# Optimization experiments

Measured on AMD Instinct MI355X. Metric: run time of the kernel, lower is better.

Reference implementation:

```python
import jax, jax.numpy as jnp
import numpy as np

NQ, NT, NA = 10000, 50000, 50000
E_GR, E_LT, E_SIM, E_COMP, E_GEN = 50000, 50000, 80000, 100000, 50000
HID, NH, HC, DOT, NL = 512, 4, 128, 256, 2
NEG_SLOPE = 0.2  # PyG GATv2Conv default negative_slope


def _gatv2(x_src, x_dst, src, dst, Wl, bl, Wr, br, att, bias, n_dst):
    # GATv2: x_j = lin_l(x_src), x_i = lin_r(x_dst); e = att . leaky_relu(x_i + x_j)
    xl = (x_src @ Wl + bl).reshape(-1, NH, HC)   # [Ns,H,C]
    xr = (x_dst @ Wr + br).reshape(-1, NH, HC)   # [Nd,H,C]
    m = jax.nn.leaky_relu(xl[src] + xr[dst], NEG_SLOPE)      # [E,H,C]
    logits = jnp.einsum('ehc,hc->eh', m, att)                # [E,H]
    lmax = jax.lax.stop_gradient(jax.ops.segment_max(logits, dst, num_segments=n_dst))
    lmax = jnp.where(jnp.isfinite(lmax), lmax, 0.0)
    ex = jnp.exp(logits - lmax[dst])
    denom = jax.ops.segment_sum(ex, dst, num_segments=n_dst)
    alpha = ex / (denom[dst] + 1e-16)                        # softmax over incoming edges
    out = jax.ops.segment_sum(xl[src] * alpha[:, :, None], dst, num_segments=n_dst)
    return out.reshape(n_dst, NH * HC) + bias


def _layernorm(x, g, b):
    mu = x.mean(-1, keepdims=True)
    var = ((x - mu) ** 2).mean(-1, keepdims=True)
    return (x - mu) / jnp.sqrt(var + 1e-5) * g + b


def _forward(xq, xt, xa, answer_features,
             qp_W, qp_b, tp_W, tp_b, ap_W, ap_b,
             afp_W1, afp_b1, afp_W2, afp_b2,
             conv_Wl, conv_bl, conv_Wr, conv_br, conv_att, conv_bias,
             qh_W, qh_b, qh_g, qh_beta, rh_W, rh_b, rh_g, rh_beta, score_bias,
             ei_gr, ei_lt, ei_sim, ei_comp, ei_gen):
    hq = xq @ qp_W + qp_b
    ht = xt @ tp_W + tp_b
    ha = xa @ ap_W + ap_b
    # add_self_loops=True only for ('query','similar_to','query')
    loops = jnp.arange(NQ, dtype=ei_sim.dtype)
    sim_src = jnp.concatenate([ei_sim[0], loops])
    sim_dst = jnp.concatenate([ei_sim[1], loops])
    for l in range(NL):
        P = lambda r: (conv_Wl[l, r], conv_bl[l, r], conv_Wr[l, r], conv_br[l, r], conv_att[l, r], conv_bias[l, r])
        o_gr = _gatv2(hq, ht, ei_gr[0], ei_gr[1], *P(0), NT)          # query -> think
        o_rgr = _gatv2(ht, hq, ei_gr[1], ei_gr[0], *P(1), NQ)         # think -> query (rev)
        o_lt = _gatv2(ht, ha, ei_lt[0], ei_lt[1], *P(2), NA)          # think -> answer
        o_rlt = _gatv2(ha, ht, ei_lt[1], ei_lt[0], *P(3), NT)         # answer -> think (rev)
        o_sim = _gatv2(hq, hq, sim_src, sim_dst, *P(4), NQ)           # query -> query
        o_cmp = _gatv2(ht, ht, ei_comp[0], ei_comp[1], *P(5), NT)     # think -> think
        # HeteroConv aggr='mean' across relations per destination type, then relu
        hq = jax.nn.relu((o_rgr + o_sim) / 2.0)
        ht = jax.nn.relu((o_gr + o_rlt + o_cmp) / 3.0)
        ha = jax.nn.relu(o_lt)
    q_emb = hq[ei_gen[0]]
    a_emb = ha[ei_gen[1]]
    t_emb = ht[ei_gen[1]]  # faithful to source: think indexed with answer-side index
    af_emb = jax.nn.relu(answer_features @ afp_W1 + afp_b1) @ afp_W2 + afp_b2
    q = _layernorm(q_emb @ qh_W + qh_b, qh_g, qh_beta)
    r = _layernorm(jnp.concatenate([t_emb, a_emb, af_emb], -1) @ rh_W + rh_b, rh_g, rh_beta)
    return (q * r).sum(-1) / jnp.sqrt(jnp.float32(DOT)) + score_bias


def setup_inputs() -> dict:
    ks = jax.random.split(jax.random.key(0), 40)
    n = lambda j, shape, s=0.05: jax.random.normal(ks[j], shape, jnp.float32) * s
    ri = lambda j, shape, hi: jax.random.randint(ks[j], shape, 0, hi, jnp.int32)
    return dict(
        xq=n(0, (NQ, 384), 1.0), xt=n(1, (NT, 384), 1.0), xa=n(2, (NA, 384), 1.0),
        answer_features=n(3, (E_GEN, 6), 1.0),
        qp_W=n(4, (384, HID)), qp_b=n(5, (HID,)),
        tp_W=n(6, (384, HID)), tp_b=n(7, (HID,)),
        ap_W=n(8, (384, HID)), ap_b=n(9, (HID,)),
        afp_W1=n(10, (6, 64)), afp_b1=n(11, (64,)),
        afp_W2=n(12, (64, HID)), afp_b2=n(13, (HID,)),
        conv_Wl=n(14, (NL, 6, HID, HID)), conv_bl=n(15, (NL, 6, HID)),
        conv_Wr=n(16, (NL, 6, HID, HID)), conv_br=n(17, (NL, 6, HID)),
        conv_att=n(18, (NL, 6, NH, HC)), conv_bias=n(19, (NL, 6, HID)),
        qh_W=n(20, (HID, DOT)), qh_b=n(21, (DOT,)),
        qh_g=jnp.ones((DOT,), jnp.float32), qh_beta=jnp.zeros((DOT,), jnp.float32),
        rh_W=n(22, (HID * 3, DOT)), rh_b=n(23, (DOT,)),
        rh_g=jnp.ones((DOT,), jnp.float32), rh_beta=jnp.zeros((DOT,), jnp.float32),
        score_bias=jnp.zeros((1,), jnp.float32),
        ei_gr=jnp.stack([ri(24, (E_GR,), NQ), ri(25, (E_GR,), NT)]),
        ei_lt=jnp.stack([ri(26, (E_LT,), NT), ri(27, (E_LT,), NA)]),
        ei_sim=ri(28, (2, E_SIM), NQ),
        ei_comp=ri(29, (2, E_COMP), NT),
        ei_gen=jnp.stack([ri(30, (E_GEN,), NQ), ri(31, (E_GEN,), NA)]),
    )


def reference(xq, xt, xa, answer_features,
              qp_W, qp_b, tp_W, tp_b, ap_W, ap_b,
              afp_W1, afp_b1, afp_W2, afp_b2,
              conv_Wl, conv_bl, conv_Wr, conv_br, conv_att, conv_bias,
              qh_W, qh_b, qh_g, qh_beta, rh_W, rh_b, rh_g, rh_beta, score_bias,
              ei_gr, ei_lt, ei_sim, ei_comp, ei_gen):
    return _forward(xq, xt, xa, answer_features,
                    qp_W, qp_b, tp_W, tp_b, ap_W, ap_b,
                    afp_W1, afp_b1, afp_W2, afp_b2,
                    conv_Wl, conv_bl, conv_Wr, conv_br, conv_att, conv_bias,
                    qh_W, qh_b, qh_g, qh_beta, rh_W, rh_b, rh_g, rh_beta, score_bias,
                    ei_gr, ei_lt, ei_sim, ei_comp, ei_gen)
```

## Files before the change

kernel.cpp:

```cpp
#include <hip/hip_runtime.h>
#include <cstdio>
#include <type_traits>

#define NQ 10000
#define NT 50000
#define NA 50000
#define E_GR 50000
#define E_LT 50000
#define E_SIM 80000
#define E_COMP 100000
#define E_GEN 50000
#define NEG_SLOPE 0.2f

#define NDTOT 220000
#define NSTOT 220000
#define ETOT  390000
__device__ __constant__ const int c_degOff[7]  = {0, 50000, 60000, 110000, 120000, 170000, 220000};
__device__ __constant__ const int c_sOff[7]    = {0, 10000, 60000, 110000, 120000, 170000, 220000};
__device__ __constant__ const int c_eOff[7]    = {0, 50000, 100000, 150000, 240000, 340000, 390000};

typedef unsigned short bf16_t;
typedef unsigned int u32;
typedef __attribute__((ext_vector_type(8))) short short8v;
typedef __attribute__((ext_vector_type(4))) float f32x4;

__device__ __forceinline__ float bf2f(u32 bits) { return __uint_as_float(bits << 16); }
__device__ __forceinline__ u32 f2bf(float f) {
  u32 u = __float_as_uint(f);
  return (u + 0x7FFFu + ((u >> 16) & 1u)) >> 16;
}
__device__ __forceinline__ u32 pack2(float a, float b) { return f2bf(a) | (f2bf(b) << 16); }
__device__ __forceinline__ void unpack8(uint4 u, float* f) {
  f[0] = bf2f(u.x & 0xffffu); f[1] = bf2f(u.x >> 16);
  f[2] = bf2f(u.y & 0xffffu); f[3] = bf2f(u.y >> 16);
  f[4] = bf2f(u.z & 0xffffu); f[5] = bf2f(u.z >> 16);
  f[6] = bf2f(u.w & 0xffffu); f[7] = bf2f(u.w >> 16);
}

__device__ __forceinline__ void gload16(const void* g, void* l) {
  __builtin_amdgcn_global_load_lds(
      (const __attribute__((address_space(1))) void*)g,
      (__attribute__((address_space(3))) void*)l, 16, 0, 0);
}

struct GemmDesc {
  const bf16_t* A; const bf16_t* Bt; const float* bias; void* C;
  const int* ridx; int N; const int* Nc; int K;
};

template <typename CT>
__global__ __launch_bounds__(512, 4) void bgemm(
    GemmDesc d0, GemmDesc d1, GemmDesc d2, int M, int accumulate)
{
  __shared__ short lds[3][12288];
  const int z = blockIdx.z;
  GemmDesc d = (z == 2) ? d2 : (z == 1) ? d1 : d0;
  int N = d.Nc ? *d.Nc : d.N;
  const int K = d.K;

  const int tid = threadIdx.x;
  const int ncol = gridDim.x;
  const int nband = (N + 127) >> 7;
  int lin = blockIdx.y * ncol + blockIdx.x;
  if (lin >= ncol * nband) return;

  int band, col;
  const int full = (nband >> 3) * 8 * ncol;
  if (lin < full) {
    int g = lin >> 3, x = lin & 7;
    band = x + 8 * (g / ncol);
    col  = g % ncol;
  } else {
    int r = lin - full;
    band = (nband & ~7) + r / ncol;
    col  = r % ncol;
  }
  const int bm = band * 128, bn = col * 256;

  const int lane = tid & 63;
  const int w = tid >> 6;
  const int wr = w >> 2, wc = w & 3;
  const int fr = lane & 15, fg = lane >> 4;

  const int kg = (((tid & 3) ^ ((tid >> 3) & 3)) << 3);
  const int rr = tid >> 2;
  int ra = min(bm + rr, N - 1);
  const bf16_t* gA0 = d.A + (size_t)(d.ridx ? d.ridx[ra] : ra) * K + kg;
  const bf16_t* gB0 = d.Bt + (size_t)(bn + rr) * K + kg;
  const bf16_t* gB1 = d.Bt + (size_t)(bn + 128 + rr) * K + kg;
  const int wb = w << 9;

  f32x4 acc[4][4];
#pragma unroll
  for (int i = 0; i < 4; ++i)
#pragma unroll
    for (int j = 0; j < 4; ++j) acc[i][j] = (f32x4){0.f, 0.f, 0.f, 0.f};

  auto stage = [&](int buf, int k0) {
    short* base = &lds[buf][0];
    gload16(gA0 + k0, base + wb);
    gload16(gB0 + k0, base + 4096 + wb);
    gload16(gB1 + k0, base + 8192 + wb);
  };

  const int nsteps = K >> 5;
  stage(0, 0);
  const int co = (fg ^ ((fr >> 1) & 3)) << 3;
  for (int s = 0; s < nsteps; ++s) {
    const int cur = s % 3;
    if (s + 1 < nsteps) {
      stage((s + 1) % 3, (s + 1) << 5);
      asm volatile("s_waitcnt vmcnt(3)" ::: "memory");
    } else {
      asm volatile("s_waitcnt vmcnt(0)" ::: "memory");
    }
    __builtin_amdgcn_s_barrier();
    asm volatile("" ::: "memory");
    const short* LA = &lds[cur][0];
    const short* LB = &lds[cur][4096];
    short8v b[4];
#pragma unroll
    for (int j = 0; j < 4; ++j) {
      int R = wc * 64 + j * 16 + fr;
      b[j] = *(const short8v*)&LB[R * 32 + co];
    }
#pragma unroll
    for (int i = 0; i < 4; ++i) {
      int R = wr * 64 + i * 16 + fr;
      short8v a = *(const short8v*)&LA[R * 32 + co];
#pragma unroll
      for (int j = 0; j < 4; ++j)
        acc[i][j] = __builtin_amdgcn_mfma_f32_16x16x32_bf16(b[j], a,
                                                            acc[i][j], 0, 0, 0);
    }
    asm volatile("" ::: "memory");
  }

  CT* C = (CT*)d.C;
  float4 bv[4];
#pragma unroll
  for (int j = 0; j < 4; ++j) {
    bv[j] = make_float4(0.f, 0.f, 0.f, 0.f);
    if (!accumulate && d.bias)
      bv[j] = *(const float4*)(d.bias + bn + wc * 64 + j * 16 + fg * 4);
  }
#pragma unroll
  for (int i = 0; i < 4; ++i) {
    const int n = bm + wr * 64 + i * 16 + fr;
    if (n >= N) continue;
#pragma unroll
    for (int j = 0; j < 4; ++j) {
      const int m0 = bn + wc * 64 + j * 16 + fg * 4;
      f32x4 v = acc[i][j];
      if constexpr (std::is_same<CT, float>::value) {
        float* p = C + (size_t)n * M + m0;
        if (accumulate) {
          float4 o = *(float4*)p;
          o.x += v[0]; o.y += v[1]; o.z += v[2]; o.w += v[3];
          *(float4*)p = o;
        } else {
          *(float4*)p = make_float4(v[0] + bv[j].x, v[1] + bv[j].y,
                                    v[2] + bv[j].z, v[3] + bv[j].w);
        }
      } else {
        uint2 o;
        o.x = pack2(v[0] + bv[j].x, v[1] + bv[j].y);
        o.y = pack2(v[2] + bv[j].z, v[3] + bv[j].w);
        *(uint2*)(C + (size_t)n * M + m0) = o;
      }
    }
  }
}

__device__ __forceinline__ void wT_tile(
    const float* __restrict__ W, bf16_t* __restrict__ Wt, int K, int M)
{
  __shared__ float sm[32][33];
  int mb = blockIdx.x * 32, kb = blockIdx.y * 32;
  int tx = threadIdx.x & 31, ty = threadIdx.x >> 5;
#pragma unroll
  for (int i = 0; i < 4; ++i)
    sm[ty + i * 8][tx] = W[(size_t)(kb + ty + i * 8) * M + mb + tx];
  __syncthreads();
#pragma unroll
  for (int i = 0; i < 4; ++i)
    Wt[(size_t)(mb + ty + i * 8) * K + kb + tx] = (bf16_t)f2bf(sm[tx][ty + i * 8]);
}

__global__ __launch_bounds__(256) void convert_wT(
    const float* __restrict__ W, bf16_t* __restrict__ Wt, int K, int M)
{
  wT_tile(W + (size_t)blockIdx.z * K * M, Wt + (size_t)blockIdx.z * K * M, K, M);
}
__global__ __launch_bounds__(256) void convert_wT24(
    const float* __restrict__ Wl, bf16_t* __restrict__ wl,
    const float* __restrict__ Wr, bf16_t* __restrict__ wr)
{
  int z = blockIdx.z;
  size_t o = (size_t)(z < 12 ? z : z - 12) * 512 * 512;
  if (z < 12) wT_tile(Wl + o, wl + o, 512, 512);
  else        wT_tile(Wr + o, wr + o, 512, 512);
}
__global__ __launch_bounds__(256) void convert_wT3(
    const float* __restrict__ W0, const float* __restrict__ W1,
    const float* __restrict__ W2, bf16_t* __restrict__ T0,
    bf16_t* __restrict__ T1, bf16_t* __restrict__ T2)
{
  int z = blockIdx.z;
  const float* W = z == 0 ? W0 : z == 1 ? W1 : W2;
  bf16_t* T = z == 0 ? T0 : z == 1 ? T1 : T2;
  wT_tile(W, T, 384, 512);
}
__global__ __launch_bounds__(256) void convert_wT4h(
    const float* __restrict__ qh, const float* __restrict__ rh,
    bf16_t* __restrict__ wqh, bf16_t* __restrict__ wrh)
{
  int z = blockIdx.z;
  if (z == 0) wT_tile(qh, wqh, 512, 256);
  else        wT_tile(rh + (size_t)(z - 1) * 512 * 256,
                      wrh + (size_t)(z - 1) * 256 * 512, 512, 256);
}

__global__ __launch_bounds__(256) void cast_flat(
    const float* __restrict__ in, bf16_t* __restrict__ out, int n4)
{
  int t = blockIdx.x * 256 + threadIdx.x;
  if (t >= n4) return;
  float4 v = ((const float4*)in)[t];
  uint2 o;
  o.x = pack2(v.x, v.y);
  o.y = pack2(v.z, v.w);
  ((uint2*)out)[t] = o;
}

__global__ __launch_bounds__(256) void fold_cvec(
    const float* __restrict__ b2, const float* __restrict__ rh2,
    float* __restrict__ cvec)
{
  int m = threadIdx.x;
  float s = 0.f;
  for (int k = 0; k < 512; ++k) s = fmaf(b2[k], rh2[(size_t)k * 256 + m], s);
  cvec[m] = s;
}

#define N4_XQ (NQ * 96)
#define N4_XT (NT * 96)
#define N4_XA (NA * 96)
__global__ __launch_bounds__(256) void cast3(
    const float* __restrict__ xq, const float* __restrict__ xt,
    const float* __restrict__ xa, bf16_t* __restrict__ xqb,
    bf16_t* __restrict__ xtb, bf16_t* __restrict__ xab)
{
  long g = (long)blockIdx.x * 256 + threadIdx.x;
  const float* in; bf16_t* out; long idx;
  if (g < N4_XQ)                { in = xq; out = xqb; idx = g; }
  else if (g < N4_XQ + N4_XT)   { in = xt; out = xtb; idx = g - N4_XQ; }
  else if (g < N4_XQ + N4_XT + N4_XA) { in = xa; out = xab; idx = g - N4_XQ - N4_XT; }
  else return;
  float4 v = ((const float4*)in)[idx];
  uint2 o;
  o.x = pack2(v.x, v.y);
  o.y = pack2(v.z, v.w);
  ((uint2*)out)[idx] = o;
}

__global__ __launch_bounds__(256) void combine_bias6(
    const float* __restrict__ cb, float* __restrict__ bcAll)
{
  int g = blockIdx.x * 256 + threadIdx.x;
  if (g >= 6 * 512) return;
  int row = g >> 9, j = g & 511;
  int l = row / 3, kind = row % 3;
  const float* b = cb + (size_t)l * 6 * 512;
  float v;
  if (kind == 0)      v = (b[0 * 512 + j] + b[3 * 512 + j] + b[5 * 512 + j]) / 3.f;
  else if (kind == 1) v = (b[1 * 512 + j] + b[4 * 512 + j]) * 0.5f;
  else                v = b[2 * 512 + j];
  bcAll[(size_t)row * 512 + j] = v;
}

__device__ __forceinline__ int find_rel6(int g, const int* off) {
  int r = 0;
#pragma unroll
  for (int k = 1; k < 6; ++k) r += (g >= off[k]);
  return r;
}

__global__ __launch_bounds__(256) void hist6(
    const int* __restrict__ d0, const int* __restrict__ d1,
    const int* __restrict__ d2, const int* __restrict__ d3,
    const int* __restrict__ d4, const int* __restrict__ d5,
    const int* __restrict__ s0p, const int* __restrict__ s1p,
    const int* __restrict__ s2p, const int* __restrict__ s3p,
    const int* __restrict__ s4p, const int* __restrict__ s5p,
    int* __restrict__ degAll, int* __restrict__ sdegAll, int* __restrict__ pos)
{
  int g = blockIdx.x * 256 + threadIdx.x;
  if (g >= ETOT) return;
  int r = find_rel6(g, c_eOff);
  int le = g - c_eOff[r];
  const int* dp = r == 0 ? d0 : r == 1 ? d1 : r == 2 ? d2 : r == 3 ? d3
                : r == 4 ? d4 : d5;
  const int* sp = r == 0 ? s0p : r == 1 ? s1p : r == 2 ? s2p : r == 3 ? s3p
                : r == 4 ? s4p : s5p;
  pos[g] = atomicAdd(&degAll[c_degOff[r] + dp[le]], 1);
  atomicAdd(&sdegAll[c_sOff[r] + sp[le]], 1);
}

__global__ __launch_bounds__(256) void scanAll(
    const int* __restrict__ degAll, const int* __restrict__ sdegAll,
    int* __restrict__ startAll, int* __restrict__ cposAll,
    int* __restrict__ sposAll, int* __restrict__ ccount, int* __restrict__ scount)
{
  __shared__ int sm[256];
  int b = blockIdx.x;
  int j = b / 6, r = b % 6;
  const int* dOff = (j == 2) ? c_sOff : c_degOff;
  const int* in   = (j == 2) ? sdegAll : degAll;
  int* out = j == 0 ? startAll : j == 1 ? cposAll : sposAll;
  int base0 = dOff[r], n = dOff[r + 1] - base0;
  int t = threadIdx.x;
  int carry = 0;
  for (int c0 = 0; c0 < n; c0 += 1024) {
    int base = c0 + t * 4;
    int v[4], sum = 0;
#pragma unroll
    for (int k = 0; k < 4; ++k) {
      int raw = (base + k < n) ? in[base0 + base + k] : 0;
      v[k] = j == 0 ? raw : j == 1 ? (raw >= 2 ? 1 : 0) : (raw >= 1 ? 1 : 0);
      sum += v[k];
    }
    sm[t] = sum;
    __syncthreads();
    for (int off = 1; off < 256; off <<= 1) {
      int x = (t >= off) ? sm[t - off] : 0;
      __syncthreads();
      sm[t] += x;
      __syncthreads();
    }
    int run = carry + (t > 0 ? sm[t - 1] : 0);
#pragma unroll
    for (int k = 0; k < 4; ++k) {
      if (base + k < n) out[base0 + base + k] = run;
      run += v[k];
    }
    carry += sm[255];
    __syncthreads();
  }
  if (t == 0) {
    if (j == 1) ccount[r] = carry;
    if (j == 2) scount[r] = carry;
  }
}

__global__ __launch_bounds__(256) void scatter6(
    const int* __restrict__ d0, const int* __restrict__ d1,
    const int* __restrict__ d2, const int* __restrict__ d3,
    const int* __restrict__ d4, const int* __restrict__ d5,
    const int* __restrict__ s0p, const int* __restrict__ s1p,
    const int* __restrict__ s2p, const int* __restrict__ s3p,
    const int* __restrict__ s4p, const int* __restrict__ s5p,
    const int* __restrict__ startAll, const int* __restrict__ pos,
    const int* __restrict__ sposAll,
    int* __restrict__ eidxAll, int* __restrict__ srcCAll)
{
  int g = blockIdx.x * 256 + threadIdx.x;
  if (g >= ETOT) return;
  int r = find_rel6(g, c_eOff);
  int le = g - c_eOff[r];
  const int* dp = r == 0 ? d0 : r == 1 ? d1 : r == 2 ? d2 : r == 3 ? d3
                : r == 4 ? d4 : d5;
  const int* sp = r == 0 ? s0p : r == 1 ? s1p : r == 2 ? s2p : r == 3 ? s3p
                : r == 4 ? s4p : s5p;
  eidxAll[c_eOff[r] + startAll[c_degOff[r] + dp[le]] + pos[g]] = le;
  srcCAll[g] = sposAll[c_sOff[r] + sp[le]];
}

__global__ __launch_bounds__(256) void compactBoth(
    const int* __restrict__ degAll, const int* __restrict__ cposAll,
    int* __restrict__ cidxAll,
    const int* __restrict__ sdegAll, const int* __restrict__ sposAll,
    int* __restrict__ sidxAll)
{
  int g = blockIdx.x * 256 + threadIdx.x;
  if (g < NDTOT) {
    if (degAll[g] >= 2) {
      int r = find_rel6(g, c_degOff);
      cidxAll[c_degOff[r] + cposAll[g]] = g - c_degOff[r];
    }
  } else if (g < NDTOT + NSTOT) {
    int h = g - NDTOT;
    if (sdegAll[h] >= 1) {
      int r = find_rel6(h, c_sOff);
      sidxAll[c_sOff[r] + sposAll[h]] = h - c_sOff[r];
    }
  }
}

__global__ __launch_bounds__(256) void gat_fused(
    const bf16_t* __restrict__ xl, const bf16_t* __restrict__ xr,
    const int* __restrict__ srcC, const int* __restrict__ start,
    const int* __restrict__ deg, const int* __restrict__ eidx,
    const int* __restrict__ cpos, const float* __restrict__ att,
    bf16_t* __restrict__ acc, int Nd, int accumulate,
    const float* __restrict__ bc, float inv_div)
{
  int d = blockIdx.x * 4 + (threadIdx.x >> 6);
  if (d >= Nd) return;
  int lane = threadIdx.x & 63;

  float acc8[8] = {0.f, 0.f, 0.f, 0.f, 0.f, 0.f, 0.f, 0.f};
  int n = deg[d], s0 = start[d];
  if (n == 1) {
    int s = srcC[eidx[s0]];
    unpack8(*(const uint4*)(xl + (size_t)s * 512 + lane * 8), acc8);
  } else if (n > 1) {
    float xrr[8];
    unpack8(*(const uint4*)(xr + (size_t)cpos[d] * 512 + lane * 8), xrr);
    float at[8];
    *(float4*)(at)     = *(const float4*)(att + lane * 8);
    *(float4*)(at + 4) = *(const float4*)(att + lane * 8 + 4);
    float den = 0.f;
    int sN = srcC[eidx[s0]];
    for (int i = 0; i < n; ++i) {
      int s = sN;
      if (i + 1 < n) sN = srcC[eidx[s0 + i + 1]];
      float f[8];
      unpack8(*(const uint4*)(xl + (size_t)s * 512 + lane * 8), f);
      float p = 0.f;
#pragma unroll
      for (int k = 0; k < 8; ++k) {
        float x = f[k] + xrr[k];
        p = fmaf(at[k], x >= 0.f ? x : NEG_SLOPE * x, p);
      }
#pragma unroll
      for (int m = 8; m >= 1; m >>= 1) p += __shfl_xor(p, m);
      float ex = __expf(p);
      den += ex;
#pragma unroll
      for (int k = 0; k < 8; ++k) acc8[k] = fmaf(ex, f[k], acc8[k]);
    }
    float inv = 1.f / (den + 1e-16f);
#pragma unroll
    for (int k = 0; k < 8; ++k) acc8[k] *= inv;
  }

  bf16_t* out = acc + (size_t)d * 512 + lane * 8;
  if (accumulate) {
    float old[8];
    unpack8(*(const uint4*)out, old);
#pragma unroll
    for (int k = 0; k < 8; ++k) acc8[k] += old[k];
  }
  if (bc) {
    float bcv[8];
    *(float4*)(bcv)     = *(const float4*)(bc + lane * 8);
    *(float4*)(bcv + 4) = *(const float4*)(bc + lane * 8 + 4);
#pragma unroll
    for (int k = 0; k < 8; ++k)
      acc8[k] = fmaxf(fmaf(acc8[k], inv_div, bcv[k]), 0.f);
  }
  uint4 s;
  s.x = pack2(acc8[0], acc8[1]); s.y = pack2(acc8[2], acc8[3]);
  s.z = pack2(acc8[4], acc8[5]); s.w = pack2(acc8[6], acc8[7]);
  *(uint4*)out = s;
}

__global__ __launch_bounds__(256) void af_hidden(
    const float* __restrict__ af, const float* __restrict__ W1,
    const float* __restrict__ b1, bf16_t* __restrict__ out, int n)
{
  int t = blockIdx.x * blockDim.x + threadIdx.x;
  if (t >= n * 64) return;
  int i = t >> 6, j = t & 63;
  const float* a = af + (size_t)i * 6;
  float s = b1[j];
#pragma unroll
  for (int k = 0; k < 6; ++k) s = fmaf(a[k], W1[k * 64 + j], s);
  out[t] = (bf16_t)f2bf(fmaxf(s, 0.f));
}

__global__ __launch_bounds__(256) void build_sim(
    const int* __restrict__ ei, int* __restrict__ ss, int* __restrict__ sd)
{
  int t = blockIdx.x * blockDim.x + threadIdx.x;
  if (t >= E_SIM + NQ) return;
  if (t < E_SIM) { ss[t] = ei[t]; sd[t] = ei[E_SIM + t]; }
  else           { ss[t] = t - E_SIM; sd[t] = t - E_SIM; }
}

__global__ __launch_bounds__(256) void head_final(
    const float* __restrict__ qn, const float* __restrict__ rn,
    const float* __restrict__ afr, const float* __restrict__ cvec,
    const int* __restrict__ gsrc, const int* __restrict__ gdst,
    const float* __restrict__ qg, const float* __restrict__ qb,
    const float* __restrict__ rg, const float* __restrict__ rb,
    const float* __restrict__ score_bias, float* __restrict__ out, int E)
{
  int e = blockIdx.x * 4 + (threadIdx.x >> 6);
  if (e >= E) return;
  int lane = threadIdx.x & 63;

  float4 q = *(const float4*)(qn + (size_t)gsrc[e] * 256 + lane * 4);
  float s = q.x + q.y + q.z + q.w;
#pragma unroll
  for (int m = 32; m >= 1; m >>= 1) s += __shfl_xor(s, m);
  float mu = s * (1.f / 256.f);
  float dq0 = q.x - mu, dq1 = q.y - mu, dq2 = q.z - mu, dq3 = q.w - mu;
  float v = dq0 * dq0 + dq1 * dq1 + dq2 * dq2 + dq3 * dq3;
#pragma unroll
  for (int m = 32; m >= 1; m >>= 1) v += __shfl_xor(v, m);
  float rstd = rsqrtf(v * (1.f / 256.f) + 1e-5f);
  float4 g4 = *(const float4*)(qg + lane * 4);
  float4 b4 = *(const float4*)(qb + lane * 4);
  float qn0 = dq0 * rstd * g4.x + b4.x, qn1 = dq1 * rstd * g4.y + b4.y;
  float qn2 = dq2 * rstd * g4.z + b4.z, qn3 = dq3 * rstd * g4.w + b4.w;

  float4 r0 = *(const float4*)(rn + (size_t)gdst[e] * 256 + lane * 4);
  float4 r1 = *(const float4*)(afr + (size_t)e * 256 + lane * 4);
  float4 cv = *(const float4*)(cvec + lane * 4);
  float4 r;
  r.x = r0.x + r1.x + cv.x;
  r.y = r0.y + r1.y + cv.y;
  r.z = r0.z + r1.z + cv.z;
  r.w = r0.w + r1.w + cv.w;
  s = r.x + r.y + r.z + r.w;
#pragma unroll
  for (int m = 32; m >= 1; m >>= 1) s += __shfl_xor(s, m);
  mu = s * (1.f / 256.f);
  float dr0 = r.x - mu, dr1 = r.y - mu, dr2 = r.z - mu, dr3 = r.w - mu;
  v = dr0 * dr0 + dr1 * dr1 + dr2 * dr2 + dr3 * dr3;
#pragma unroll
  for (int m = 32; m >= 1; m >>= 1) v += __shfl_xor(v, m);
  rstd = rsqrtf(v * (1.f / 256.f) + 1e-5f);
  g4 = *(const float4*)(rg + lane * 4);
  b4 = *(const float4*)(rb + lane * 4);
  float rn0 = dr0 * rstd * g4.x + b4.x, rn1 = dr1 * rstd * g4.y + b4.y;
  float rn2 = dr2 * rstd * g4.z + b4.z, rn3 = dr3 * rstd * g4.w + b4.w;

  float d = qn0 * rn0 + qn1 * rn1 + qn2 * rn2 + qn3 * rn3;
#pragma unroll
  for (int m = 32; m >= 1; m >>= 1) d += __shfl_xor(d, m);
  if (lane == 0) out[e] = d * 0.0625f + score_bias[0];
}

extern "C" void kernel_launch(void* const* d_in, const int* in_sizes, int n_in,
                              void* d_out, int out_size, void* d_ws, size_t ws_size,
                              hipStream_t stream) {
  (void)in_sizes; (void)n_in; (void)out_size;
  const float* xq      = (const float*)d_in[0];
  const float* xt      = (const float*)d_in[1];
  const float* xa      = (const float*)d_in[2];
  const float* af      = (const float*)d_in[3];
  const float* qp_W    = (const float*)d_in[4];
  const float* qp_b    = (const float*)d_in[5];
  const float* tp_W    = (const float*)d_in[6];
  const float* tp_b    = (const float*)d_in[7];
  const float* ap_W    = (const float*)d_in[8];
  const float* ap_b    = (const float*)d_in[9];
  const float* afp_W1  = (const float*)d_in[10];
  const float* afp_b1  = (const float*)d_in[11];
  const float* afp_W2  = (const float*)d_in[12];
  const float* afp_b2  = (const float*)d_in[13];
  const float* conv_Wl = (const float*)d_in[14];
  const float* conv_bl = (const float*)d_in[15];
  const float* conv_Wr = (const float*)d_in[16];
  const float* conv_br = (const float*)d_in[17];
  const float* conv_att  = (const float*)d_in[18];
  const float* conv_bias = (const float*)d_in[19];
  const float* qh_W    = (const float*)d_in[20];
  const float* qh_b    = (const float*)d_in[21];
  const float* qh_g    = (const float*)d_in[22];
  const float* qh_beta = (const float*)d_in[23];
  const float* rh_W    = (const float*)d_in[24];
  const float* rh_b    = (const float*)d_in[25];
  const float* rh_g    = (const float*)d_in[26];
  const float* rh_beta = (const float*)d_in[27];
  const float* score_b = (const float*)d_in[28];
  const int* ei_gr   = (const int*)d_in[29];
  const int* ei_lt   = (const int*)d_in[30];
  const int* ei_sim  = (const int*)d_in[31];
  const int* ei_comp = (const int*)d_in[32];
  const int* ei_gen  = (const int*)d_in[33];

  char* base = (char*)d_ws;
  size_t off = 0;
  auto alloc = [&](size_t bytes) {
    void* p = base + off;
    off = (off + bytes + 255) & ~(size_t)255;
    return p;
  };
  bf16_t* hq   = (bf16_t*)alloc((size_t)NQ * 512 * 2);
  bf16_t* ht   = (bf16_t*)alloc((size_t)NT * 512 * 2);
  bf16_t* ha   = (bf16_t*)alloc((size_t)NA * 512 * 2);
  bf16_t* acct = (bf16_t*)alloc((size_t)NT * 512 * 2);
  bf16_t* accq = (bf16_t*)alloc((size_t)NQ * 512 * 2);
  bf16_t* xlb  = (bf16_t*)alloc((size_t)50000 * 512 * 2);
  bf16_t* xrb  = (bf16_t*)alloc((size_t)50000 * 512 * 2);
  int* simsrc  = (int*)alloc((size_t)(E_SIM + NQ) * 4);
  int* simdst  = (int*)alloc((size_t)(E_SIM + NQ) * 4);

  bf16_t* wqp  = (bf16_t*)alloc((size_t)512 * 384 * 2);
  bf16_t* wtp  = (bf16_t*)alloc((size_t)512 * 384 * 2);
  bf16_t* wap  = (bf16_t*)alloc((size_t)512 * 384 * 2);
  bf16_t* wl   = (bf16_t*)alloc((size_t)12 * 512 * 512 * 2);
  bf16_t* wr   = (bf16_t*)alloc((size_t)12 * 512 * 512 * 2);
  bf16_t* wqh  = (bf16_t*)alloc((size_t)256 * 512 * 2);
  bf16_t* wrh0 = (bf16_t*)alloc((size_t)256 * 512 * 2);
  bf16_t* wrh1 = (bf16_t*)alloc((size_t)256 * 512 * 2);
  bf16_t* wrh2 = (bf16_t*)alloc((size_t)256 * 512 * 2);
  float* bcAll = (float*)alloc(6 * 512 * 4);
  bf16_t* a2b    = (bf16_t*)alloc((size_t)64 * 512 * 2);
  float*  wfoldF = (float*)alloc((size_t)64 * 256 * 4);
  bf16_t* wfoldT = (bf16_t*)alloc((size_t)256 * 64 * 2);
  float*  cvec   = (float*)alloc(256 * 4);

  int* degAll   = (int*)alloc((size_t)NDTOT * 4);
  int* sdegAll  = (int*)alloc((size_t)NSTOT * 4);
  int* startAll = (int*)alloc((size_t)NDTOT * 4);
  int* cposAll  = (int*)alloc((size_t)NDTOT * 4);
  int* cidxAll  = (int*)alloc((size_t)NDTOT * 4);
  int* sposAll  = (int*)alloc((size_t)NSTOT * 4);
  int* sidxAll  = (int*)alloc((size_t)NSTOT * 4);
  int* eidxAll  = (int*)alloc((size_t)ETOT * 4);
  int* srcCAll  = (int*)alloc((size_t)ETOT * 4);
  int* posb     = (int*)alloc((size_t)ETOT * 4);
  int* ccount   = (int*)alloc(6 * 4);
  int* scount   = (int*)alloc(6 * 4);
  if (off > ws_size) {
    fprintf(stderr, "kernel_launch: ws too small, need %zu have %zu\n", off, ws_size);
    return;
  }

  const int degOff[6] = {0, 50000, 60000, 110000, 120000, 170000};
  const int sOff[6]   = {0, 10000, 60000, 110000, 120000, 170000};
  const int eOff[6]   = {0, 50000, 100000, 150000, 240000, 340000};

  auto mkDesc = [](const bf16_t* A, const bf16_t* Bt, const float* bias, void* C,
                   const int* ridx, int N, const int* Nc, int K) {
    GemmDesc d; d.A = A; d.Bt = Bt; d.bias = bias; d.C = C;
    d.ridx = ridx; d.N = N; d.Nc = Nc; d.K = K; return d;
  };
  GemmDesc dz = mkDesc(nullptr, nullptr, nullptr, nullptr, nullptr, 0, nullptr, 32);

  auto launch_b = [&](GemmDesc a, GemmDesc b, GemmDesc c, int nz, int maxN,
                      int M, int acc_) {
    dim3 g(M / 256, (maxN + 127) / 128, nz);
    bgemm<bf16_t><<<g, 512, 0, stream>>>(a, b, c, M, acc_);
  };
  auto launch_f = [&](GemmDesc a, GemmDesc b, GemmDesc c, int nz, int maxN,
                      int M, int acc_) {
    dim3 g(M / 256, (maxN + 127) / 128, nz);
    bgemm<float><<<g, 512, 0, stream>>>(a, b, c, M, acc_);
  };

  convert_wT24<<<dim3(16, 16, 24), 256, 0, stream>>>(conv_Wl, wl, conv_Wr, wr);
  convert_wT3<<<dim3(16, 12, 3), 256, 0, stream>>>(qp_W, tp_W, ap_W, wqp, wtp, wap);
  convert_wT4h<<<dim3(8, 16, 4), 256, 0, stream>>>(qh_W, rh_W, wqh, wrh0);
  combine_bias6<<<(6 * 512 + 255) / 256, 256, 0, stream>>>(conv_bias, bcAll);
  cast_flat<<<(64 * 512 / 4 + 255) / 256, 256, 0, stream>>>(afp_W2, a2b, 64 * 512 / 4);
  launch_f(mkDesc(a2b, wrh2, nullptr, wfoldF, nullptr, 64, nullptr, 512),
           dz, dz, 1, 64, 256, 0);
  convert_wT<<<dim3(8, 2, 1), 256, 0, stream>>>(wfoldF, wfoldT, 64, 256);
  fold_cvec<<<1, 256, 0, stream>>>(afp_b2, rh_W + 1024 * 256, cvec);

  build_sim<<<(E_SIM + NQ + 255) / 256, 256, 0, stream>>>(ei_sim, simsrc, simdst);
  const int* dsts[6]  = {ei_gr + E_GR, ei_gr, ei_lt, simdst,
                         ei_comp + E_COMP, ei_lt + E_LT};
  const int* srcsA[6] = {ei_gr, ei_gr + E_GR, ei_lt + E_LT, simsrc,
                         ei_comp, ei_lt};
  hipMemsetAsync(degAll, 0, (size_t)(sdegAll + NSTOT) - (size_t)degAll, stream);
  hist6<<<(ETOT + 255) / 256, 256, 0, stream>>>(
      dsts[0], dsts[1], dsts[2], dsts[3], dsts[4], dsts[5],
      srcsA[0], srcsA[1], srcsA[2], srcsA[3], srcsA[4], srcsA[5],
      degAll, sdegAll, posb);
  scanAll<<<18, 256, 0, stream>>>(degAll, sdegAll, startAll, cposAll, sposAll,
                                  ccount, scount);
  scatter6<<<(ETOT + 255) / 256, 256, 0, stream>>>(
      dsts[0], dsts[1], dsts[2], dsts[3], dsts[4], dsts[5],
      srcsA[0], srcsA[1], srcsA[2], srcsA[3], srcsA[4], srcsA[5],
      startAll, posb, sposAll, eidxAll, srcCAll);
  compactBoth<<<(NDTOT + NSTOT + 255) / 256, 256, 0, stream>>>(
      degAll, cposAll, cidxAll, sdegAll, sposAll, sidxAll);

  cast3<<<((long)(N4_XQ + N4_XT + N4_XA) + 255) / 256, 256, 0, stream>>>(
      xq, xt, xa, accq, xlb, xrb);
  launch_b(mkDesc(accq, wqp, qp_b, hq, nullptr, NQ, nullptr, 384),
           mkDesc(xlb, wtp, tp_b, ht, nullptr, NT, nullptr, 384),
           mkDesc(xrb, wap, ap_b, ha, nullptr, NA, nullptr, 384),
           3, NT, 512, 0);

  const int NdArr[6] = {NT, NQ, NT, NQ, NT, NA};
  const int NsArr[6] = {NQ, NT, NA, NQ, NT, NT};
  bf16_t *hq_i = hq, *ht_i = ht, *hq_o = accq, *ht_o = acct;
  for (int l = 0; l < 2; ++l) {
    const float* bc_t = bcAll + (size_t)(l * 3 + 0) * 512;
    const float* bc_q = bcAll + (size_t)(l * 3 + 1) * 512;
    const float* bc_a = bcAll + (size_t)(l * 3 + 2) * 512;

    struct Rel { const bf16_t* xs; const bf16_t* xd; int po; bf16_t* acc;
                 int accum; const float* bc; float inv; };
    Rel rels[6] = {
      {hq_i, ht_i, 0, ht_o, 0, nullptr, 0.f},
      {ht_i, hq_i, 1, hq_o, 0, nullptr, 0.f},
      {ha,   ht_i, 3, ht_o, 1, nullptr, 0.f},
      {hq_i, hq_i, 4, hq_o, 1, bc_q, 0.5f},
      {ht_i, ht_i, 5, ht_o, 1, bc_t, 1.f / 3.f},
      {ht_i, ha,   2, ha,   0, bc_a, 1.f},
    };
    for (int r = 0; r < 6; ++r) {
      const Rel& R = rels[r];
      int Nd_ = NdArr[r];
      size_t po = (size_t)l * 6 + R.po;
      int maxN = NsArr[r] > Nd_ ? NsArr[r] : Nd_;
      launch_b(mkDesc(R.xs, wl + po * 512 * 512, conv_bl + po * 512, xlb,
                      sidxAll + sOff[r], NsArr[r], scount + r, 512),
               mkDesc(R.xd, wr + po * 512 * 512, conv_br + po * 512, xrb,
                      cidxAll + degOff[r], Nd_, ccount + r, 512),
               dz, 2, maxN, 512, 0);
      int gb = (Nd_ + 3) / 4;
      gat_fused<<<gb, 256, 0, stream>>>(xlb, xrb, srcCAll + eOff[r],
                                        startAll + degOff[r], degAll + degOff[r],
                                        eidxAll + eOff[r], cposAll + degOff[r],
                                        conv_att + po * 512,
                                        R.acc, Nd_, R.accum, R.bc, R.inv);
    }
    bf16_t* t;
    t = hq_i; hq_i = hq_o; hq_o = t;
    t = ht_i; ht_i = ht_o; ht_o = t;
  }

  float* qn  = (float*)accq;
  float* rn  = (float*)acct;
  float* afr = (float*)xrb;
  bf16_t* afh = xlb;
  const int* gsrc = ei_gen;
  const int* gdst = ei_gen + E_GEN;

  af_hidden<<<(E_GEN * 64 + 255) / 256, 256, 0, stream>>>(af, afp_W1, afp_b1,
                                                          afh, E_GEN);
  launch_f(mkDesc(hq_i, wqh, qh_b, qn, nullptr, NQ, nullptr, 512),
           mkDesc(ht_i, wrh0, rh_b, rn, nullptr, NT, nullptr, 512),
           mkDesc(afh, wfoldT, nullptr, afr, nullptr, E_GEN, nullptr, 64),
           3, NT, 256, 0);
  launch_f(mkDesc(ha, wrh1, nullptr, rn, nullptr, NA, nullptr, 512),
           dz, dz, 1, NA, 256, 1);
  head_final<<<(E_GEN + 3) / 4, 256, 0, stream>>>(
      qn, rn, afr, cvec, gsrc, gdst,
      qh_g, qh_beta, rh_g, rh_beta, score_b, (float*)d_out, E_GEN);
}
```

Measured before the change: 1.255 ms.

## Split serial per-relation prefix scan into three-pass parallel block scan

After: 1.192 ms. -5.0%, faster.

```diff
diff --git a/kernel.cpp b/kernel.cpp
--- a/kernel.cpp
+++ b/kernel.cpp
@@ -18,6 +18,10 @@
 __device__ __constant__ const int c_degOff[7]  = {0, 50000, 60000, 110000, 120000, 170000, 220000};
 __device__ __constant__ const int c_sOff[7]    = {0, 10000, 60000, 110000, 120000, 170000, 220000};
 __device__ __constant__ const int c_eOff[7]    = {0, 50000, 100000, 150000, 240000, 340000, 390000};
+__device__ __constant__ const int c_nb[6]      = {49, 10, 49, 10, 49, 49};
+__device__ __constant__ const int c_nbOff[7]   = {0, 49, 59, 108, 118, 167, 216};
+__device__ __constant__ const int c_snb[6]     = {10, 49, 49, 10, 49, 49};
+__device__ __constant__ const int c_snbOff[7]  = {0, 10, 59, 108, 118, 167, 216};
 
 typedef unsigned short bf16_t;
 typedef unsigned int u32;
@@ -307,50 +311,83 @@
   atomicAdd(&sdegAll[c_sOff[r] + sp[le]], 1);
 }
 
-__global__ __launch_bounds__(256) void scanAll(
+__global__ __launch_bounds__(256) void scan1All(
     const int* __restrict__ degAll, const int* __restrict__ sdegAll,
     int* __restrict__ startAll, int* __restrict__ cposAll,
-    int* __restrict__ sposAll, int* __restrict__ ccount, int* __restrict__ scount)
+    int* __restrict__ sposAll, int* __restrict__ bsumAll)
 {
   __shared__ int sm[256];
-  int b = blockIdx.x;
-  int j = b / 6, r = b % 6;
-  const int* dOff = (j == 2) ? c_sOff : c_degOff;
-  const int* in   = (j == 2) ? sdegAll : degAll;
+  int j = blockIdx.x / 216, bb = blockIdx.x % 216;
+  const int* nbOff = (j == 2) ? c_snbOff : c_nbOff;
+  const int* dOff  = (j == 2) ? c_sOff : c_degOff;
+  const int* in    = (j == 2) ? sdegAll : degAll;
   int* out = j == 0 ? startAll : j == 1 ? cposAll : sposAll;
+  int r = 0;
+#pragma unroll
+  for (int k = 1; k < 6; ++k) r += (bb >= nbOff[k]);
+  int lb = bb - nbOff[r];
   int base0 = dOff[r], n = dOff[r + 1] - base0;
   int t = threadIdx.x;
-  int carry = 0;
-  for (int c0 = 0; c0 < n; c0 += 1024) {
-    int base = c0 + t * 4;
-    int v[4], sum = 0;
-#pragma unroll
-    for (int k = 0; k < 4; ++k) {
-      int raw = (base + k < n) ? in[base0 + base + k] : 0;
-      v[k] = j == 0 ? raw : j == 1 ? (raw >= 2 ? 1 : 0) : (raw >= 1 ? 1 : 0);
-      sum += v[k];
-    }
-    sm[t] = sum;
+  int base = lb * 1024 + t * 4;
+  int v[4], sum = 0;
+#pragma unroll
+  for (int k = 0; k < 4; ++k) {
+    int raw = (base + k < n) ? in[base0 + base + k] : 0;
+    v[k] = j == 0 ? raw : j == 1 ? (raw >= 2 ? 1 : 0) : (raw >= 1 ? 1 : 0);
+    sum += v[k];
+  }
+  sm[t] = sum;
+  __syncthreads();
+  for (int off = 1; off < 256; off <<= 1) {
+    int x = (t >= off) ? sm[t - off] : 0;
     __syncthreads();
-    for (int off = 1; off < 256; off <<= 1) {
-      int x = (t >= off) ? sm[t - off] : 0;
-      __syncthreads();
-      sm[t] += x;
-      __syncthreads();
-    }
-    int run = carry + (t > 0 ? sm[t - 1] : 0);
-#pragma unroll
-    for (int k = 0; k < 4; ++k) {
-      if (base + k < n) out[base0 + base + k] = run;
-      run += v[k];
-    }
-    carry += sm[255];
+    sm[t] += x;
     __syncthreads();
   }
-  if (t == 0) {
-    if (j == 1) ccount[r] = carry;
-    if (j == 2) scount[r] = carry;
-  }
+  int run = (t > 0) ? sm[t - 1] : 0;
+  if (t == 255) bsumAll[j * 384 + r * 64 + lb] = sm[255];
+#pragma unroll
+  for (int k = 0; k < 4; ++k) {
+    if (base + k < n) out[base0 + base + k] = run;
+    run += v[k];
+  }
+}
+
+__global__ __launch_bounds__(64) void scan2All(
+    int* __restrict__ bsumAll, int* __restrict__ ccount, int* __restrict__ scount)
+{
+  __shared__ int sm[64];
+  int j = blockIdx.x / 6, r = blockIdx.x % 6;
+  int nb = (j == 2) ? c_snb[r] : c_nb[r];
+  int t = threadIdx.x;
+  int v = (t < nb) ? bsumAll[j * 384 + r * 64 + t] : 0;
+  sm[t] = v;
+  __syncthreads();
+  for (int off = 1; off < 64; off <<= 1) {
+    int x = (t >= off) ? sm[t - off] : 0;
+    __syncthreads();
+    sm[t] += x;
+    __syncthreads();
+  }
+  if (t < nb) bsumAll[j * 384 + r * 64 + t] = sm[t] - v;
+  if (t == nb - 1) {
+    if (j == 1) ccount[r] = sm[t];
+    if (j == 2) scount[r] = sm[t];
+  }
+}
+
+__global__ __launch_bounds__(256) void scan3All(
+    int* __restrict__ startAll, int* __restrict__ cposAll,
+    int* __restrict__ sposAll, const int* __restrict__ bsumAll)
+{
+  int g = blockIdx.x * 256 + threadIdx.x;
+  if (g >= 3 * NDTOT) return;
+  int j = g / NDTOT, ln0 = g % NDTOT;
+  const int* dOff = (j == 2) ? c_sOff : c_degOff;
+  int* out = j == 0 ? startAll : j == 1 ? cposAll : sposAll;
+  int r = find_rel6(ln0, dOff);
+  int ln = ln0 - dOff[r];
+  out[ln0] += bsumAll[j * 384 + r * 64 + (ln >> 10)];
 }
 
 __global__ __launch_bounds__(256) void scatter6(
@@ -625,6 +662,7 @@
   int* eidxAll  = (int*)alloc((size_t)ETOT * 4);
   int* srcCAll  = (int*)alloc((size_t)ETOT * 4);
   int* posb     = (int*)alloc((size_t)ETOT * 4);
+  int* bsumAll  = (int*)alloc(3 * 6 * 64 * 4);
   int* ccount   = (int*)alloc(6 * 4);
   int* scount   = (int*)alloc(6 * 4);
   if (off > ws_size) {
@@ -674,8 +712,11 @@
       dsts[0], dsts[1], dsts[2], dsts[3], dsts[4], dsts[5],
       srcsA[0], srcsA[1], srcsA[2], srcsA[3], srcsA[4], srcsA[5],
       degAll, sdegAll, posb);
-  scanAll<<<18, 256, 0, stream>>>(degAll, sdegAll, startAll, cposAll, sposAll,
-                                  ccount, scount);
+  scan1All<<<648, 256, 0, stream>>>(degAll, sdegAll, startAll, cposAll,
+                                    sposAll, bsumAll);
+  scan2All<<<18, 64, 0, stream>>>(bsumAll, ccount, scount);
+  scan3All<<<(3 * NDTOT + 255) / 256, 256, 0, stream>>>(startAll, cposAll,
+                                                        sposAll, bsumAll);
   scatter6<<<(ETOT + 255) / 256, 256, 0, stream>>>(
       dsts[0], dsts[1], dsts[2], dsts[3], dsts[4], dsts[5],
       srcsA[0], srcsA[1], srcsA[2], srcsA[3], srcsA[4], srcsA[5],
```
